# Kernel optimization log

Hardware: AMD Instinct MI355X
Metric: run time of the kernel (lower is better)

The kernel has to match this reference:

```python
import jax, jax.numpy as jnp
import numpy as np

DIM = 1024
HEADS = 16
HDIM = DIM // HEADS
MLP_HID = 4096
LN_EPS = 1e-5
NORM_EPS = 1e-12  # F.normalize eps


def _layernorm(x, g, b):
    mu = jnp.mean(x, axis=-1, keepdims=True)
    var = jnp.mean(jnp.square(x - mu), axis=-1, keepdims=True)
    return (x - mu) / jnp.sqrt(var + LN_EPS) * g + b


def _l2norm(x):
    n = jnp.linalg.norm(x, axis=-1, keepdims=True)
    return x / jnp.maximum(n, NORM_EPS)


def setup_inputs() -> dict:
    key = jax.random.key(0)
    ks = jax.random.split(key, 8)
    s = 0.02
    x = jax.random.normal(ks[0], (2, 2048, DIM), dtype=jnp.float32)
    w_qkv = jax.random.normal(ks[1], (3 * DIM, DIM), dtype=jnp.float32) * s  # torch Linear weight (out,in)
    w_proj = jax.random.normal(ks[2], (DIM, DIM), dtype=jnp.float32) * s
    temp = jnp.ones((HEADS, 1, 1), dtype=jnp.float32)
    w1 = jax.random.normal(ks[3], (MLP_HID, DIM), dtype=jnp.float32) * s
    b1 = jnp.zeros((MLP_HID,), dtype=jnp.float32)
    w2 = jax.random.normal(ks[4], (DIM, MLP_HID), dtype=jnp.float32) * s
    b2 = jnp.zeros((DIM,), dtype=jnp.float32)
    ln1_g = jnp.ones((DIM,), dtype=jnp.float32)
    ln1_b = jnp.zeros((DIM,), dtype=jnp.float32)
    ln2_g = jnp.ones((DIM,), dtype=jnp.float32)
    ln2_b = jnp.zeros((DIM,), dtype=jnp.float32)
    return {"x": x, "ln1_g": ln1_g, "ln1_b": ln1_b, "w_qkv": w_qkv,
            "w_proj": w_proj, "temp": temp, "ln2_g": ln2_g, "ln2_b": ln2_b,
            "w1": w1, "b1": b1, "w2": w2, "b2": b2}


def reference(x, ln1_g, ln1_b, w_qkv, w_proj, temp, ln2_g, ln2_b, w1, b1, w2, b2):
    b, n, c = x.shape
    # --- MHSA with L2-normalized q,k and learnable per-head temperature ---
    h = _layernorm(x, ln1_g, ln1_b)
    qkv = h @ w_qkv.T                             # [b,n,3c]
    qkv = qkv.reshape(b, n, 3, HEADS, HDIM).transpose(2, 0, 3, 1, 4)  # [3,b,h,n,d]
    q, k, v = qkv[0], qkv[1], qkv[2]
    q = _l2norm(q)
    k = _l2norm(k)
    attn = jnp.einsum('bhnd,bhmd->bhnm', q, k) * temp  # temp [h,1,1] broadcasts
    attn = jax.nn.softmax(attn, axis=-1)
    out = jnp.einsum('bhnm,bhmd->bhnd', attn, v)       # [b,h,n,d]
    out = out.transpose(0, 2, 1, 3).reshape(b, n, c)
    x = x + out @ w_proj.T
    # --- MLP ---
    h = _layernorm(x, ln2_g, ln2_b)
    h = jax.nn.gelu(h @ w1.T + b1, approximate=False)
    x = x + h @ w2.T + b2
    return x
```

## Files before the change

### kernel.cpp

```cpp
#include <hip/hip_runtime.h>
#include <cstdint>
#include <cstddef>

typedef unsigned short u16;
typedef __attribute__((ext_vector_type(8))) short short8;
typedef __attribute__((ext_vector_type(4))) float f32x4;
typedef __attribute__((ext_vector_type(4))) float float4v;
typedef __attribute__((ext_vector_type(4))) u16 u16x4;

__device__ __forceinline__ u16 f2bf(float f) {
  union { float f; uint32_t u; } v; v.f = f;
  uint32_t u = v.u;
  return (u16)((u + 0x7FFFu + ((u >> 16) & 1u)) >> 16);
}
__device__ __forceinline__ float bf2f(u16 s) {
  union { uint32_t u; float f; } v; v.u = ((uint32_t)s) << 16; return v.f;
}

__device__ __forceinline__ float fast_exp2(float x) {
#if __has_builtin(__builtin_amdgcn_exp2f)
  return __builtin_amdgcn_exp2f(x);
#else
  return exp2f(x);
#endif
}

__device__ __forceinline__ void gload16(const u16* g, u16* l) {
  __builtin_amdgcn_global_load_lds((const __attribute__((address_space(1))) void*)g,
                                   (__attribute__((address_space(3))) void*)l,
                                   16, 0, 0);
}

#define SBAR __builtin_amdgcn_sched_barrier(0)

__global__ __launch_bounds__(256) void k_cvt4(const float* __restrict__ wqkv, const float* __restrict__ wproj,
                                              const float* __restrict__ w1, const float* __restrict__ w2,
                                              u16* __restrict__ o_qkv, u16* __restrict__ o_proj,
                                              u16* __restrict__ o_w1, u16* __restrict__ o_w2) {
  const int total = 3145728;
  int stride = gridDim.x * 256;
  for (int i = blockIdx.x * 256 + threadIdx.x; i < total; i += stride) {
    const float* src; u16* dst; int loc;
    if (i < 786432)       { src = wqkv;  dst = o_qkv;  loc = i; }
    else if (i < 1048576) { src = wproj; dst = o_proj; loc = i - 786432; }
    else if (i < 2097152) { src = w1;    dst = o_w1;   loc = i - 1048576; }
    else                  { src = w2;    dst = o_w2;   loc = i - 2097152; }
    float4v v = *(const float4v*)(src + (size_t)loc * 4);
    u16x4 o;
    #pragma unroll
    for (int j = 0; j < 4; j++) o[j] = f2bf(v[j]);
    *(u16x4*)(dst + (size_t)loc * 4) = o;
  }
}

__global__ __launch_bounds__(256) void k_ln(const float* __restrict__ x, const float* __restrict__ g,
                                            const float* __restrict__ b, u16* __restrict__ out) {
  int row = blockIdx.x, tid = threadIdx.x;
  int wid = tid >> 6;
  const float* xr = x + (size_t)row * 1024;
  float4v v = *(const float4v*)(xr + tid * 4);
  float s = v[0] + v[1] + v[2] + v[3];
  float sq = v[0]*v[0] + v[1]*v[1] + v[2]*v[2] + v[3]*v[3];
  #pragma unroll
  for (int m = 1; m <= 32; m <<= 1) { s += __shfl_xor(s, m); sq += __shfl_xor(sq, m); }
  __shared__ float ss[4], ssq[4];
  if ((tid & 63) == 0) { ss[wid] = s; ssq[wid] = sq; }
  __syncthreads();
  s = ss[0] + ss[1] + ss[2] + ss[3];
  sq = ssq[0] + ssq[1] + ssq[2] + ssq[3];
  float mu = s * (1.0f/1024.0f);
  float var = sq * (1.0f/1024.0f) - mu*mu;
  float rs = rsqrtf(var + 1e-5f);
  u16x4 o;
  #pragma unroll
  for (int j = 0; j < 4; j++) {
    float y = (v[j] - mu) * rs * g[tid*4+j] + b[tid*4+j];
    o[j] = f2bf(y);
  }
  *(u16x4*)(out + (size_t)row * 1024 + tid * 4) = o;
}

__global__ __launch_bounds__(256) void k_redln(const float* __restrict__ x, const u16* __restrict__ P,
                                               const float* __restrict__ g, const float* __restrict__ b,
                                               float* __restrict__ x1, u16* __restrict__ h2) {
  int row = blockIdx.x, tid = threadIdx.x;
  int wid = tid >> 6;
  size_t off = (size_t)row * 1024 + tid * 4;
  float4v v = *(const float4v*)(x + off);
  #pragma unroll
  for (int z = 0; z < 4; z++) {
    u16x4 p = *(const u16x4*)(P + (size_t)z * 4194304 + off);
    #pragma unroll
    for (int j = 0; j < 4; j++) v[j] += bf2f(p[j]);
  }
  *(float4v*)(x1 + off) = v;
  float s = v[0] + v[1] + v[2] + v[3];
  float sq = v[0]*v[0] + v[1]*v[1] + v[2]*v[2] + v[3]*v[3];
  #pragma unroll
  for (int m = 1; m <= 32; m <<= 1) { s += __shfl_xor(s, m); sq += __shfl_xor(sq, m); }
  __shared__ float ss[4], ssq[4];
  if ((tid & 63) == 0) { ss[wid] = s; ssq[wid] = sq; }
  __syncthreads();
  s = ss[0] + ss[1] + ss[2] + ss[3];
  sq = ssq[0] + ssq[1] + ssq[2] + ssq[3];
  float mu = s * (1.0f/1024.0f);
  float var = sq * (1.0f/1024.0f) - mu*mu;
  float rs = rsqrtf(var + 1e-5f);
  u16x4 o;
  #pragma unroll
  for (int j = 0; j < 4; j++) o[j] = f2bf((v[j] - mu) * rs * g[tid*4+j] + b[tid*4+j]);
  *(u16x4*)(h2 + off) = o;
}

template<int EPI>
__global__ __launch_bounds__(512, 2) void k_g256(const u16* __restrict__ A, const u16* __restrict__ B,
                                                 const float* __restrict__ bias, u16* __restrict__ Cb,
                                                 int M, int N, int K, int Ksub) {
  extern __shared__ __align__(16) u16 smem[];
  int tid = threadIdx.x;
  int gx = gridDim.x;
  int lin = blockIdx.y * gx + blockIdx.x;
  int nwg = gx * gridDim.y;
  int cpx = nwg >> 3;
  int swz = (lin & 7) * cpx + (lin >> 3);
  int bx = swz % gx, by = swz / gx;
  int m0 = by * 256, n0 = bx * 256;
  int kbase = blockIdx.z * Ksub;
  int wid = tid >> 6, lane = tid & 63;
  int wm = wid >> 2, wn = wid & 3;
  int l15 = lane & 15, l16 = lane >> 4;

  f32x4 acc[8][4] = {};
  int nt = Ksub >> 6;

  auto STAGE = [&](int bsel, int kb) {
    #pragma unroll
    for (int st = 0; st < 2; st++) {
      u16* abase = smem + bsel*32768 + st*16384;
      u16* bbase = abase + 8192;
      int kbs = kb + st*32;
      #pragma unroll
      for (int i = 0; i < 2; i++) {
        int c = i*512 + tid;
        int R = c >> 3, p = c & 7;
        int sp = p ^ (R & 7);
        int r = 2*R + (sp >> 2);
        int g = sp & 3;
        gload16(A + (size_t)(m0 + r)*K + kbs + g*8, abase + c*8);
        gload16(B + (size_t)(n0 + r)*K + kbs + g*8, bbase + c*8);
      }
    }
  };

  STAGE(0, kbase);

  for (int t = 0; t < nt; ++t) {
    int sl = t & 1;
    asm volatile("s_waitcnt vmcnt(0)" ::: "memory");
    SBAR;
    __builtin_amdgcn_s_barrier();
    SBAR;
    if (t + 1 < nt) STAGE(sl ^ 1, kbase + (t + 1) * 64);
    #pragma unroll
    for (int st = 0; st < 2; st++) {
      const u16* ab = smem + sl*32768 + st*16384;
      const u16* bb = ab + 8192;
      short8 af[8], bf[4];
      #pragma unroll
      for (int mf = 0; mf < 8; mf++) {
        int r = wm*128 + mf*16 + l15;
        int R = r >> 1;
        int sp = ((r & 1)*4 + l16) ^ (R & 7);
        af[mf] = *(const short8*)(ab + R*64 + sp*8);
      }
      #pragma unroll
      for (int nf = 0; nf < 4; nf++) {
        int r = wn*64 + nf*16 + l15;
        int R = r >> 1;
        int sp = ((r & 1)*4 + l16) ^ (R & 7);
        bf[nf] = *(const short8*)(bb + R*64 + sp*8);
      }
      asm volatile("s_waitcnt lgkmcnt(0)" ::: "memory");
      SBAR;
      __builtin_amdgcn_s_setprio(1);
      #pragma unroll
      for (int mf = 0; mf < 8; mf++)
        #pragma unroll
        for (int nf = 0; nf < 4; nf++)
          acc[mf][nf] = __builtin_amdgcn_mfma_f32_16x16x32_bf16(af[mf], bf[nf], acc[mf][nf], 0, 0, 0);
      __builtin_amdgcn_s_setprio(0);
    }
  }

  size_t zoff = (EPI == 6) ? (size_t)blockIdx.z * M * N : 0;
  #pragma unroll
  for (int mf = 0; mf < 8; mf++) {
    #pragma unroll
    for (int nf = 0; nf < 4; nf++) {
      int col = n0 + wn*64 + nf*16 + l15;
      #pragma unroll
      for (int r = 0; r < 4; r++) {
        int row = m0 + wm*128 + mf*16 + l16*4 + r;
        float v = acc[mf][nf][r];
        if constexpr (EPI == 2) { v += bias[col]; v = 0.5f*v*(1.0f + erff(v*0.70710678118f)); }
        Cb[zoff + (size_t)row*N + col] = f2bf(v);
      }
    }
  }
}

template<int NP, int HASB>
__global__ __launch_bounds__(256) void k_red(const float* __restrict__ base, const float* __restrict__ bias,
                                             const u16* __restrict__ P, size_t zstride, float* __restrict__ out) {
  int i = blockIdx.x * 256 + threadIdx.x;
  float4v v = *(const float4v*)(base + (size_t)i * 4);
  if constexpr (HASB) {
    float4v bb = *(const float4v*)(bias + (size_t)(i & 255) * 4);
    #pragma unroll
    for (int j = 0; j < 4; j++) v[j] += bb[j];
  }
  #pragma unroll
  for (int z = 0; z < NP; z++) {
    u16x4 p = *(const u16x4*)(P + (size_t)z * zstride + (size_t)i * 4);
    #pragma unroll
    for (int j = 0; j < 4; j++) v[j] += bf2f(p[j]);
  }
  *(float4v*)(out + (size_t)i * 4) = v;
}

__global__ __launch_bounds__(256) void k_prep(const u16* __restrict__ qkv, const float* __restrict__ temp,
                                              u16* __restrict__ Qn, u16* __restrict__ Kn, u16* __restrict__ Vt) {
  int grp = blockIdx.x, bh = blockIdx.y;
  int b = bh >> 4, h = bh & 15;
  int tid = threadIdx.x;
  int n0 = grp * 64;
  __shared__ __align__(16) u16 vs[64*64];
  float tmp = temp[h] * 1.44269504f;
  int j8 = tid & 7;
  #pragma unroll
  for (int pass = 0; pass < 2; pass++) {
    int tl = pass*32 + (tid >> 3);
    size_t roff = (size_t)((b*2048) + n0 + tl) * 3072 + h*64 + j8*8;
    short8 q8 = *(const short8*)(qkv + roff);
    short8 k8 = *(const short8*)(qkv + roff + 1024);
    short8 v8 = *(const short8*)(qkv + roff + 2048);
    float qv[8], kv[8];
    float sq = 0.f, sk = 0.f;
    #pragma unroll
    for (int jj = 0; jj < 8; jj++) {
      qv[jj] = bf2f((u16)q8[jj]); sq += qv[jj]*qv[jj];
      kv[jj] = bf2f((u16)k8[jj]); sk += kv[jj]*kv[jj];
    }
    sq += __shfl_xor(sq, 1); sq += __shfl_xor(sq, 2); sq += __shfl_xor(sq, 4);
    sk += __shfl_xor(sk, 1); sk += __shfl_xor(sk, 2); sk += __shfl_xor(sk, 4);
    float qs = tmp / fmaxf(sqrtf(sq), 1e-12f);
    float ksc = 1.0f / fmaxf(sqrtf(sk), 1e-12f);
    short8 qo, ko;
    #pragma unroll
    for (int jj = 0; jj < 8; jj++) {
      qo[jj] = (short)f2bf(qv[jj] * qs);
      ko[jj] = (short)f2bf(kv[jj] * ksc);
    }
    size_t obase = ((size_t)bh*2048 + n0 + tl)*64 + j8*8;
    *(short8*)(Qn + obase) = qo;
    *(short8*)(Kn + obase) = ko;
    *(short8*)&vs[tl*64 + j8*8] = v8;
  }
  __syncthreads();
  int d = tid & 63, chunk = tid >> 6;
  u16 vals[16];
  #pragma unroll
  for (int jj = 0; jj < 16; jj++) vals[jj] = vs[(chunk*16 + jj)*64 + d];
  short8 w0, w1v;
  #pragma unroll
  for (int j = 0; j < 8; j++) { w0[j] = (short)vals[j]; w1v[j] = (short)vals[8+j]; }
  size_t vo = ((size_t)bh*64 + d)*2048 + n0 + chunk*16;
  *(short8*)(Vt + vo) = w0;
  *(short8*)(Vt + vo + 8) = w1v;
}

__device__ __forceinline__ int akey(int row) { return (row & 3) | (((row >> 3) & 1) << 2); }

__global__ __launch_bounds__(256) void k_attn(const u16* __restrict__ Qn, const u16* __restrict__ Kn,
                                              const u16* __restrict__ Vt, const float* __restrict__ temp,
                                              u16* __restrict__ Out) {
  __shared__ __align__(16) u16 Ks[2][64*64];
  __shared__ __align__(16) u16 Vs[2][64*64];
  int lin = blockIdx.y * gridDim.x + blockIdx.x;
  int c = lin & 7, t5 = lin >> 3;
  int bh = c*4 + (t5 >> 4);
  int qg = t5 & 15;
  int b = bh >> 4, h = bh & 15;
  int tid = threadIdx.x, wid = tid >> 6, lane = tid & 63;
  int l15 = lane & 15, l16 = lane >> 4;
  size_t base = (size_t)bh * 2048 * 64;
  size_t vbase = (size_t)bh * 64 * 2048;
  int q0 = qg*128 + wid*32;
  float m2 = fabsf(temp[h]) * 1.44269504f;
  short8 qf[2][2];
  #pragma unroll
  for (int g = 0; g < 2; g++)
    #pragma unroll
    for (int ks = 0; ks < 2; ks++)
      qf[g][ks] = *(const short8*)(Qn + base + (size_t)(q0 + g*16 + l15)*64 + ks*32 + l16*8);
  f32x4 o[2][4] = {};
  float lrow[2] = {0.f, 0.f};
  int prow = (l15 & 3) + 8*(l15 >> 2);

  auto STAGE = [&](int bsel, int kv0) {
    #pragma unroll
    for (int i = 0; i < 2; i++) {
      int cc = i*256 + tid;
      int row = cc >> 3, p = cc & 7;
      int g = p ^ akey(row);
      gload16(Kn + base + (size_t)(kv0 + row)*64 + g*8, &Ks[bsel][(i*256 + wid*64)*8]);
      gload16(Vt + vbase + (size_t)row*2048 + kv0 + g*8, &Vs[bsel][(i*256 + wid*64)*8]);
    }
  };

  STAGE(0, 0);
  int cur = 0;
  for (int kv0 = 0; kv0 < 2048; kv0 += 64) {
    asm volatile("s_waitcnt vmcnt(0)" ::: "memory");
    SBAR;
    __builtin_amdgcn_s_barrier();
    SBAR;
    if (kv0 + 64 < 2048) STAGE(cur ^ 1, kv0 + 64);
    f32x4 s[2][4];
    #pragma unroll
    for (int g = 0; g < 2; g++)
      #pragma unroll
      for (int ss = 0; ss < 4; ss++)
        s[g][ss] = f32x4{-m2, -m2, -m2, -m2};
    __builtin_amdgcn_s_setprio(1);
    #pragma unroll
    for (int dks = 0; dks < 2; dks++) {
      #pragma unroll
      for (int ss = 0; ss < 4; ss++) {
        int row = (ss & 1)*4 + (ss >> 1)*32 + prow;
        short8 kf = *(const short8*)&Ks[cur][row*64 + ((dks*4 + l16) ^ akey(row))*8];
        s[0][ss] = __builtin_amdgcn_mfma_f32_16x16x32_bf16(kf, qf[0][dks], s[0][ss], 0, 0, 0);
        s[1][ss] = __builtin_amdgcn_mfma_f32_16x16x32_bf16(kf, qf[1][dks], s[1][ss], 0, 0, 0);
      }
    }
    __builtin_amdgcn_s_setprio(0);
    short8 pf[2][2];
    #pragma unroll
    for (int g = 0; g < 2; g++) {
      float tsum = 0.f;
      #pragma unroll
      for (int kvs = 0; kvs < 2; kvs++) {
        float e[8];
        #pragma unroll
        for (int r = 0; r < 4; r++) {
          e[r]   = fast_exp2(s[g][kvs*2][r]);
          e[4+r] = fast_exp2(s[g][kvs*2+1][r]);
        }
        #pragma unroll
        for (int r = 0; r < 8; r++) tsum += e[r];
        union { uint32_t u[4]; short8 v; } pu;
        #pragma unroll
        for (int w = 0; w < 4; w++) {
          uint32_t pk;
          asm("v_cvt_pk_bf16_f32 %0, %1, %2" : "=v"(pk) : "v"(e[2*w]), "v"(e[2*w+1]));
          pu.u[w] = pk;
        }
        pf[g][kvs] = pu.v;
      }
      lrow[g] += tsum;
    }
    __builtin_amdgcn_s_setprio(1);
    #pragma unroll
    for (int kvs = 0; kvs < 2; kvs++) {
      short8 vf[4];
      #pragma unroll
      for (int dt = 0; dt < 4; dt++) {
        int row = dt*16 + l15;
        vf[dt] = *(const short8*)&Vs[cur][row*64 + (((kvs*4 + l16) ^ akey(row))*8)];
      }
      #pragma unroll
      for (int dt = 0; dt < 4; dt++) {
        o[0][dt] = __builtin_amdgcn_mfma_f32_16x16x32_bf16(vf[dt], pf[0][kvs], o[0][dt], 0, 0, 0);
        o[1][dt] = __builtin_amdgcn_mfma_f32_16x16x32_bf16(vf[dt], pf[1][kvs], o[1][dt], 0, 0, 0);
      }
    }
    __builtin_amdgcn_s_setprio(0);
    cur ^= 1;
  }
  #pragma unroll
  for (int g = 0; g < 2; g++) {
    float l = lrow[g];
    l += __shfl_xor(l, 16);
    l += __shfl_xor(l, 32);
    float rl = 1.0f / l;
    int tok = b*2048 + q0 + g*16 + l15;
    #pragma unroll
    for (int dt = 0; dt < 4; dt++) {
      u16x4 ov;
      #pragma unroll
      for (int r = 0; r < 4; r++) ov[r] = f2bf(o[g][dt][r] * rl);
      *(u16x4*)(Out + (size_t)tok*1024 + h*64 + dt*16 + l16*4) = ov;
    }
  }
}

static constexpr size_t OFF_WQKV  = 0;
static constexpr size_t OFF_WPROJ = OFF_WQKV  + 6291456;
static constexpr size_t OFF_W1    = OFF_WPROJ + 2097152;
static constexpr size_t OFF_W2    = OFF_W1    + 8388608;
static constexpr size_t OFF_HBF   = OFF_W2    + 8388608;
static constexpr size_t OFF_QKVBF = OFF_HBF   + 8388608;
static constexpr size_t OFF_QN    = OFF_QKVBF + 25165824;
static constexpr size_t OFF_KN    = OFF_QN    + 8388608;
static constexpr size_t OFF_VT    = OFF_KN    + 8388608;
static constexpr size_t OFF_AOUT  = OFF_VT    + 8388608;
static constexpr size_t OFF_H2BF  = OFF_AOUT  + 8388608;
static constexpr size_t OFF_X1    = OFF_H2BF  + 8388608;
static constexpr size_t OFF_HID   = OFF_X1    + 16777216;

extern "C" void kernel_launch(void* const* d_in, const int* in_sizes, int n_in,
                              void* d_out, int out_size, void* d_ws, size_t ws_size,
                              hipStream_t stream) {
  (void)in_sizes; (void)n_in; (void)out_size; (void)ws_size;
  const float* x     = (const float*)d_in[0];
  const float* ln1g  = (const float*)d_in[1];
  const float* ln1b  = (const float*)d_in[2];
  const float* wqkv  = (const float*)d_in[3];
  const float* wproj = (const float*)d_in[4];
  const float* temp  = (const float*)d_in[5];
  const float* ln2g  = (const float*)d_in[6];
  const float* ln2b  = (const float*)d_in[7];
  const float* w1    = (const float*)d_in[8];
  const float* b1    = (const float*)d_in[9];
  const float* w2    = (const float*)d_in[10];
  const float* b2    = (const float*)d_in[11];

  char* ws = (char*)d_ws;
  u16* wqkv_bf  = (u16*)(ws + OFF_WQKV);
  u16* wproj_bf = (u16*)(ws + OFF_WPROJ);
  u16* w1_bf    = (u16*)(ws + OFF_W1);
  u16* w2_bf    = (u16*)(ws + OFF_W2);
  u16* h_bf     = (u16*)(ws + OFF_HBF);
  u16* h2_bf    = (u16*)(ws + OFF_H2BF);
  u16* qkv_bf   = (u16*)(ws + OFF_QKVBF);
  u16* Qn       = (u16*)(ws + OFF_QN);
  u16* Kn       = (u16*)(ws + OFF_KN);
  u16* Vt       = (u16*)(ws + OFF_VT);
  u16* aout_bf  = (u16*)(ws + OFF_AOUT);
  float* x1     = (float*)(ws + OFF_X1);
  u16* hid_bf   = (u16*)(ws + OFF_HID);
  u16* part_p   = (u16*)(ws + OFF_HID);
  u16* part_m   = (u16*)(ws + OFF_QN);
  float* outf   = (float*)d_out;

  static bool attr_done = false;
  if (!attr_done) {
    hipFuncSetAttribute((const void*)k_g256<2>, hipFuncAttributeMaxDynamicSharedMemorySize, 131072);
    hipFuncSetAttribute((const void*)k_g256<4>, hipFuncAttributeMaxDynamicSharedMemorySize, 131072);
    hipFuncSetAttribute((const void*)k_g256<6>, hipFuncAttributeMaxDynamicSharedMemorySize, 131072);
    attr_done = true;
  }

  k_cvt4<<<2048, 256, 0, stream>>>(wqkv, wproj, w1, w2, wqkv_bf, wproj_bf, w1_bf, w2_bf);

  k_ln<<<4096, 256, 0, stream>>>(x, ln1g, ln1b, h_bf);
  k_g256<4><<<dim3(12, 16), 512, 131072, stream>>>(h_bf, wqkv_bf, nullptr, qkv_bf, 4096, 3072, 1024, 1024);
  k_prep<<<dim3(32, 32), 256, 0, stream>>>(qkv_bf, temp, Qn, Kn, Vt);
  k_attn<<<dim3(16, 32), 256, 0, stream>>>(Qn, Kn, Vt, temp, aout_bf);
  k_g256<6><<<dim3(4, 16, 4), 512, 131072, stream>>>(aout_bf, wproj_bf, nullptr, part_p, 4096, 1024, 1024, 256);
  k_redln<<<4096, 256, 0, stream>>>(x, part_p, ln2g, ln2b, x1, h2_bf);
  k_g256<2><<<dim3(16, 16), 512, 131072, stream>>>(h2_bf, w1_bf, b1, hid_bf, 4096, 4096, 1024, 1024);
  k_g256<6><<<dim3(4, 16, 4), 512, 131072, stream>>>(hid_bf, w2_bf, nullptr, part_m, 4096, 1024, 4096, 1024);
  k_red<4,1><<<4096, 256, 0, stream>>>(x1, b2, part_m, 4194304, outf);
}
```

Before: 235.6 us.

## Restructure 256x256 GEMM mainloop into fine-grained quadrant ping-pong pipeline

Replaces the per-tile double-buffered loop, which waited on all loads, with a schedule that splits each 64-wide K tile into half-matrix load units. These are interleaved with quadrant-sized LDS reads and MFMA groups, and partial vmcnt waits let later tiles stream in while the current one is computed. The LDS layout also changes from paired-row packing to a row-per-64 swizzle. This adds many more barriers per iteration and assumes an even tile count (nit = ntile>>1), so odd K tile counts would drop work.

```diff
diff --git a/kernel.cpp b/kernel.cpp
--- a/kernel.cpp
+++ b/kernel.cpp
@@ -32,6 +32,10 @@
 }
 
 #define SBAR __builtin_amdgcn_sched_barrier(0)
+#define BARR_ do { SBAR; __builtin_amdgcn_s_barrier(); SBAR; } while(0)
+#define LG0_  do { asm volatile("s_waitcnt lgkmcnt(0)" ::: "memory"); SBAR; } while(0)
+#define VMW4_ do { asm volatile("s_waitcnt vmcnt(4)" ::: "memory"); SBAR; } while(0)
+#define VMW0_ do { asm volatile("s_waitcnt vmcnt(0)" ::: "memory"); SBAR; } while(0)
 
 __global__ __launch_bounds__(256) void k_cvt4(const float* __restrict__ wqkv, const float* __restrict__ wproj,
                                               const float* __restrict__ w1, const float* __restrict__ w2,
@@ -131,65 +135,88 @@
   int l15 = lane & 15, l16 = lane >> 4;
 
   f32x4 acc[8][4] = {};
-  int nt = Ksub >> 6;
-
-  auto STAGE = [&](int bsel, int kb) {
-    #pragma unroll
-    for (int st = 0; st < 2; st++) {
-      u16* abase = smem + bsel*32768 + st*16384;
-      u16* bbase = abase + 8192;
-      int kbs = kb + st*32;
-      #pragma unroll
-      for (int i = 0; i < 2; i++) {
-        int c = i*512 + tid;
-        int R = c >> 3, p = c & 7;
-        int sp = p ^ (R & 7);
-        int r = 2*R + (sp >> 2);
-        int g = sp & 3;
-        gload16(A + (size_t)(m0 + r)*K + kbs + g*8, abase + c*8);
-        gload16(B + (size_t)(n0 + r)*K + kbs + g*8, bbase + c*8);
-      }
+  int ntile = Ksub >> 6;
+  int nit = ntile >> 1;
+
+  auto UNIT = [&](int buf, int mat, int half, int kt) {
+    const u16* src = mat ? B : A;
+    int rb = (mat ? n0 : m0) + half*128;
+    u16* dstb = smem + buf*32768 + mat*16384 + half*8192;
+    #pragma unroll
+    for (int j = 0; j < 2; j++) {
+      int c = j*512 + tid;
+      int R = c >> 3, p = c & 7;
+      int g = p ^ (R & 7);
+      gload16(src + (size_t)(rb + R)*K + kbase + kt*64 + g*8, dstb + c*8);
     }
   };
-
-  STAGE(0, kbase);
-
-  for (int t = 0; t < nt; ++t) {
-    int sl = t & 1;
-    asm volatile("s_waitcnt vmcnt(0)" ::: "memory");
-    SBAR;
-    __builtin_amdgcn_s_barrier();
-    SBAR;
-    if (t + 1 < nt) STAGE(sl ^ 1, kbase + (t + 1) * 64);
-    #pragma unroll
-    for (int st = 0; st < 2; st++) {
-      const u16* ab = smem + sl*32768 + st*16384;
-      const u16* bb = ab + 8192;
-      short8 af[8], bf[4];
-      #pragma unroll
-      for (int mf = 0; mf < 8; mf++) {
-        int r = wm*128 + mf*16 + l15;
-        int R = r >> 1;
-        int sp = ((r & 1)*4 + l16) ^ (R & 7);
-        af[mf] = *(const short8*)(ab + R*64 + sp*8);
-      }
-      #pragma unroll
-      for (int nf = 0; nf < 4; nf++) {
-        int r = wn*64 + nf*16 + l15;
-        int R = r >> 1;
-        int sp = ((r & 1)*4 + l16) ^ (R & 7);
-        bf[nf] = *(const short8*)(bb + R*64 + sp*8);
-      }
-      asm volatile("s_waitcnt lgkmcnt(0)" ::: "memory");
-      SBAR;
-      __builtin_amdgcn_s_setprio(1);
-      #pragma unroll
-      for (int mf = 0; mf < 8; mf++)
+  auto RDA = [&](short8* af, int buf, int mh) {
+    const u16* ab = smem + buf*32768 + wm*8192;
+    #pragma unroll
+    for (int mf = 0; mf < 4; mf++)
+      #pragma unroll
+      for (int ks = 0; ks < 2; ks++) {
+        int lr = mh*64 + mf*16 + l15;
+        int s = (ks*4 + l16) ^ (lr & 7);
+        af[mf*2 + ks] = *(const short8*)(ab + lr*64 + s*8);
+      }
+  };
+  auto RDB = [&](short8* br, int buf, int nh) {
+    const u16* bb = smem + buf*32768 + 16384 + (wn >> 1)*8192;
+    #pragma unroll
+    for (int nf = 0; nf < 2; nf++)
+      #pragma unroll
+      for (int ks = 0; ks < 2; ks++) {
+        int lr = (wn & 1)*64 + nh*32 + nf*16 + l15;
+        int s = (ks*4 + l16) ^ (lr & 7);
+        br[nf*2 + ks] = *(const short8*)(bb + lr*64 + s*8);
+      }
+  };
+  auto QMF = [&](const short8* af, const short8* br, int mh, int nh) {
+    __builtin_amdgcn_s_setprio(1);
+    #pragma unroll
+    for (int ks = 0; ks < 2; ks++)
+      #pragma unroll
+      for (int mf = 0; mf < 4; mf++)
         #pragma unroll
-        for (int nf = 0; nf < 4; nf++)
-          acc[mf][nf] = __builtin_amdgcn_mfma_f32_16x16x32_bf16(af[mf], bf[nf], acc[mf][nf], 0, 0, 0);
-      __builtin_amdgcn_s_setprio(0);
-    }
+        for (int nf = 0; nf < 2; nf++)
+          acc[mh*4+mf][nh*2+nf] = __builtin_amdgcn_mfma_f32_16x16x32_bf16(
+              af[mf*2+ks], br[nf*2+ks], acc[mh*4+mf][nh*2+nf], 0, 0, 0);
+    __builtin_amdgcn_s_setprio(0);
+  };
+
+  UNIT(0,0,0,0); UNIT(0,0,1,0); UNIT(0,1,0,0); UNIT(0,1,1,0);
+  UNIT(1,1,0,1); UNIT(1,1,1,1);
+  VMW4_;
+  __builtin_amdgcn_s_barrier();
+  SBAR;
+
+  short8 afr[8], b0r[4], b1r[4];
+  for (int u = 0; u < nit; ++u) {
+    int tb = 2*u + 1, t2 = 2*u + 2, t3 = 2*u + 3;
+    bool has2 = (t2 < ntile), has3 = (t3 < ntile);
+    RDA(afr, 0, 0); RDB(b0r, 0, 0);
+    UNIT(1, 0, 0, tb);
+    BARR_; LG0_; QMF(afr, b0r, 0, 0); BARR_;
+    RDB(b1r, 0, 1);
+    UNIT(1, 0, 1, tb);
+    BARR_; LG0_; QMF(afr, b1r, 0, 1); BARR_;
+    RDA(afr, 0, 1);
+    if (has2) UNIT(0, 1, 0, t2);
+    BARR_; LG0_; QMF(afr, b1r, 1, 1); BARR_;
+    if (has2) { UNIT(0, 1, 1, t2); VMW4_; } else { VMW0_; }
+    BARR_; QMF(afr, b0r, 1, 0); BARR_;
+    RDA(afr, 1, 0); RDB(b0r, 1, 0);
+    if (has2) UNIT(0, 0, 0, t2);
+    BARR_; LG0_; QMF(afr, b0r, 0, 0); BARR_;
+    RDB(b1r, 1, 1);
+    if (has2) UNIT(0, 0, 1, t2);
+    BARR_; LG0_; QMF(afr, b1r, 0, 1); BARR_;
+    RDA(afr, 1, 1);
+    if (has3) UNIT(1, 1, 0, t3);
+    BARR_; LG0_; QMF(afr, b1r, 1, 1); BARR_;
+    if (has3) { UNIT(1, 1, 1, t3); VMW4_; } else { VMW0_; }
+    BARR_; QMF(afr, b0r, 1, 0); BARR_;
   }
 
   size_t zoff = (EPI == 6) ? (size_t)blockIdx.z * M * N : 0;
```

Measured after the change: 235.4 us (median of 2 runs). Within noise of the previous version (-0.1%).
